# Performance work log

Hardware: AMD Instinct MI355X
Metric: run time of the kernel (lower is better)

Reference implementation:

```python
import jax, jax.numpy as jnp
import numpy as np

NUM_TOP_QUERIES = 300
NUM_CLASSES = 80
CONF_THRESH = 0.0  # with sigmoid scores > 0 always, the mask filter is identity


def setup_inputs() -> dict:
    key = jax.random.key(0)
    k1, k2, k3 = jax.random.split(key, 3)
    N, Q, K = 256, 1000, 80
    logits = jax.random.normal(k1, (N, Q, K), dtype=jnp.float32)
    boxes = jax.random.uniform(k2, (N, Q, 4), dtype=jnp.float32)  # cxcywh in [0,1)
    original_sizes = jax.random.randint(k3, (N, 2), 1, 1333, dtype=jnp.int32)  # (h, w)
    return {"logits": logits, "boxes": boxes, "original_sizes": original_sizes}


def reference(logits, boxes, original_sizes):
    # cxcywh -> xywh (top-left x,y plus w,h)
    cxcy, wh = boxes[..., :2], boxes[..., 2:]
    boxes_xy = jnp.concatenate([cxcy - wh * 0.5, wh], axis=-1)  # (N, Q, 4)

    # NOTE: original module uses only original_sizes[0] for ALL images (faithful)
    hw = original_sizes[0]  # (h, w)
    scale = jnp.concatenate([hw[::-1], hw[::-1]]).astype(boxes.dtype)  # (w, h, w, h)
    boxes_xy = boxes_xy * scale  # (N, Q, 4)

    # sigmoid + topk over flattened (Q*K) class-query scores
    scores = jax.nn.sigmoid(logits).reshape(logits.shape[0], -1)  # (N, Q*K)
    top_scores, index = jax.lax.top_k(scores, NUM_TOP_QUERIES)  # (N, 300)

    labels = index % NUM_CLASSES          # class id
    qidx = index // NUM_CLASSES           # query id

    # gather boxes per top index: (N, 300, 4)
    gathered = jnp.take_along_axis(boxes_xy, qidx[..., None], axis=1)

    all_boxes = jnp.concatenate(
        [labels[..., None].astype(top_scores.dtype), top_scores[..., None], gathered],
        axis=-1,
    )  # (N, 300, 6)

    # Boolean confidence filter. With CONF_THRESH = 0.0 and sigmoid scores,
    # every detection is kept, so the filter+view in the original is identity.
    return all_boxes
```

## Files before the change

kernel.cpp:

```cpp
#include <hip/hip_runtime.h>

#define K_TOP  300
#define NCLS   80
#define NB     256
#define NF4    20000
#define GTHR   2.2f
#define BPB    10
#define CHUNK  2048
#define WPB    4
#define SEGC   96
#define NSEG   (BPB*WPB)
#define NCAND  (NSEG*SEGC)
#define NBK    1024

typedef unsigned int       u32;
typedef unsigned long long u64;

__device__ __forceinline__ u32 order_f32(float f) {
    u32 u = __float_as_uint(f);
    return u ^ ((u >> 31) ? 0xFFFFFFFFu : 0x80000000u);
}
__device__ __forceinline__ float unorder_f32(u32 u) {
    u32 v = (u & 0x80000000u) ? (u ^ 0x80000000u) : ~u;
    return __uint_as_float(v);
}

__device__ __forceinline__ u32 fbucket(u64 key, u32 bias14) {
    u32 d = (u32)(key >> 46) - bias14;
    return (d > 1023u) ? 1023u : d;
}

__device__ __forceinline__ u32 wstore(float v, int idx, u64* __restrict__ seg,
                                      u32 cursor, int lane) {
    const bool win = (v >= GTHR);
    const u64 mask = __ballot(win);
    if (mask) {
        if (win) {
            u32 pos = cursor + (u32)__popcll(mask & ((1ull << lane) - 1ull));
            if (pos < SEGC) {
                u32 o = order_f32(v);
                seg[pos] = ((u64)o << 32) | (u64)(0xFFFFFFFFu - (u32)idx);
            }
        }
        cursor += (u32)__popcll(mask);
    }
    return cursor;
}

__global__ __launch_bounds__(256) void collect_kernel(
    const float* __restrict__ logits,
    u32* __restrict__ gcnt,
    u64* __restrict__ gbuf)
{
    const int blk  = blockIdx.x;
    const int b    = blk & (NB - 1);
    const int c    = blk >> 8;
    const int t    = threadIdx.x;
    const int lane = t & 63;
    const int wseg = (b * BPB + c) * WPB + (t >> 6);

    const float4* __restrict__ L4 = (const float4*)(logits + (size_t)b * (NF4 * 4));
    const int base4 = c * CHUNK;

    float4 v[8];
    if (c < BPB - 1) {
        #pragma unroll
        for (int j = 0; j < 8; ++j) v[j] = L4[base4 + j * 256 + t];
    } else {
        #pragma unroll
        for (int j = 0; j < 8; ++j) {
            const int idx = base4 + j * 256 + t;
            v[j] = (idx < NF4) ? L4[idx]
                               : make_float4(-1e30f, -1e30f, -1e30f, -1e30f);
        }
    }

    u64* __restrict__ seg = gbuf + (size_t)wseg * SEGC;
    u32 cursor = 0;
    #pragma unroll
    for (int j = 0; j < 8; ++j) {
        const int i4 = (base4 + j * 256 + t) * 4;
        cursor = wstore(v[j].x, i4 + 0, seg, cursor, lane);
        cursor = wstore(v[j].y, i4 + 1, seg, cursor, lane);
        cursor = wstore(v[j].z, i4 + 2, seg, cursor, lane);
        cursor = wstore(v[j].w, i4 + 3, seg, cursor, lane);
    }
    if (lane == 0) gcnt[wseg] = cursor;
}


__device__ __forceinline__ void scan1024(u32* hist, u32* cur, u32* wsum,
                                         int* s_B, int t) {
    const int lane = t & 63, w = t >> 6;
    const u32 h = hist[t];
    u32 s = h;
    #pragma unroll
    for (int off = 1; off < 64; off <<= 1) {
        u32 v = (u32)__shfl_down((int)s, off);
        if (lane + off < 64) s += v;
    }
    if (lane == 0) wsum[w] = s;
    __syncthreads();
    u32 wexc = 0;
    #pragma unroll
    for (int j = 0; j < 16; ++j)
        if (j > w) wexc += wsum[j];
    const u32 incl = s + wexc;
    const u32 ex   = incl - h;
    if (incl >= K_TOP) atomicMax(s_B, t);
    hist[t] = ex;
    cur[t]  = ex;
}

__device__ __forceinline__ void rank_and_write(const u64* cand, const u32* hist,
                                               const u32* cur, u32 B, bool fine,
                                               u32 bias14, int t, int b,
                                               const float4* BX, float sx, float sy,
                                               float* out) {
    int total = (int)cur[B]; if (total > NCAND) total = NCAND;
    for (int i = t; i < total; i += 1024) {
        u64 key = cand[i];
        u32 bk  = fine ? fbucket(key, bias14) : (u32)(key >> 54);
        u32 o   = (u32)(key >> 32);
        u32 idx = ~((u32)key);
        int label = (int)(idx % NCLS);
        int q     = (int)(idx / NCLS);
        float4 bx = BX[q];
        int segS = (int)hist[bk];
        int segE = (int)cur[bk]; if (segE > NCAND) segE = NCAND;
        int r = segS;
        for (int j = segS; j < segE; ++j)
            r += (cand[j] > key) ? 1 : 0;
        if (r < K_TOP) {
            float logit = unorder_f32(o);
            float score = 1.0f / (1.0f + expf(-logit));
            float* po = out + ((size_t)b * K_TOP + r) * 6;
            po[0] = (float)label;
            po[1] = score;
            po[2] = (bx.x - 0.5f * bx.z) * sx;
            po[3] = (bx.y - 0.5f * bx.w) * sy;
            po[4] = bx.z * sx;
            po[5] = bx.w * sy;
        }
    }
}

__device__ void full_fallback(const float* __restrict__ logits, int b, int t,
                              u64* cand, u32* hist, u32* cur, u32* wsum, int* s_B,
                              const float4* BX, float sx, float sy,
                              float* __restrict__ out) {
    __syncthreads();
    hist[t] = 0; cur[t] = 0;
    if (t == 0) *s_B = -1;
    __syncthreads();
    const float4* L4 = (const float4*)(logits + (size_t)b * (NF4 * 4));
    for (int i = t; i < NF4; i += 1024) {
        float4 v = L4[i];
        atomicAdd(&hist[order_f32(v.x) >> 22], 1u);
        atomicAdd(&hist[order_f32(v.y) >> 22], 1u);
        atomicAdd(&hist[order_f32(v.z) >> 22], 1u);
        atomicAdd(&hist[order_f32(v.w) >> 22], 1u);
    }
    __syncthreads();
    scan1024(hist, cur, wsum, s_B, t);
    __syncthreads();
    const u32 B = (u32)*s_B;
    for (int i = t; i < NF4; i += 1024) {
        float4 v = L4[i];
        float vv[4] = {v.x, v.y, v.z, v.w};
        #pragma unroll
        for (int u2 = 0; u2 < 4; ++u2) {
            u32 o = order_f32(vv[u2]);
            u32 bk = o >> 22;
            if (bk >= B) {
                u32 pos = atomicAdd(&cur[bk], 1u);
                if (pos < NCAND)
                    cand[pos] = ((u64)o << 32) |
                                (u64)(0xFFFFFFFFu - (u32)(4*i + u2));
            }
        }
    }
    __syncthreads();
    rank_and_write(cand, hist, cur, B, false, 0u, t, b, BX, sx, sy, out);
}

__global__ __launch_bounds__(1024) void select_kernel(
    const float* __restrict__ logits,
    const float* __restrict__ boxes,
    const int*   __restrict__ osz,
    const u32*   __restrict__ gcnt,
    const u64*   __restrict__ gbuf,
    float*       __restrict__ out)
{
    __shared__ u64 cand[NCAND];
    __shared__ u32 hist[NBK];
    __shared__ u32 cur[NBK];
    __shared__ u32 wsum[16];
    __shared__ u32 scc[NSEG];
    __shared__ int s_B;

    const int b = blockIdx.x;
    const int t = threadIdx.x;
    const u64* __restrict__ gb = gbuf + (size_t)b * NCAND;
    const u32 BIAS14 = order_f32(GTHR) >> 14;

    if (t < NSEG) scc[t] = gcnt[b * NSEG + t];
    if (t == 0) s_B = -1;
    hist[t] = 0;
    __syncthreads();

    u64 k0 = 0, k1 = 0, k2 = 0, k3 = 0;
    bool v0 = false, v1 = false, v2 = false, v3 = false;
    {
        const ulonglong2* __restrict__ G2 = (const ulonglong2*)gb;
        ulonglong2 p0 = G2[t];
        int s0 = 2 * t;
        int seg0 = s0 / SEGC;
        int j0   = s0 - seg0 * SEGC;
        k0 = p0.x; k1 = p0.y;
        v0 = (j0     < (int)scc[seg0]);
        v1 = (j0 + 1 < (int)scc[seg0]);
        if (t < 896) {
            ulonglong2 p1 = G2[t + 1024];
            int s2 = 2048 + 2 * t;
            int seg2 = s2 / SEGC;
            int j2   = s2 - seg2 * SEGC;
            k2 = p1.x; k3 = p1.y;
            v2 = (j2     < (int)scc[seg2]);
            v3 = (j2 + 1 < (int)scc[seg2]);
        }
    }

    bool fast = true;
    int total = 0;
    #pragma unroll
    for (int k = 0; k < NSEG; ++k) {
        u32 x = scc[k];
        if (x > SEGC) fast = false; else total += (int)x;
    }
    fast = fast && (total >= K_TOP);

    const float sx = (float)osz[1];
    const float sy = (float)osz[0];
    const float4* BX = (const float4*)(boxes + (size_t)b * 4000);

    if (fast) {
        if (v0) atomicAdd(&hist[fbucket(k0, BIAS14)], 1u);
        if (v1) atomicAdd(&hist[fbucket(k1, BIAS14)], 1u);
        if (v2) atomicAdd(&hist[fbucket(k2, BIAS14)], 1u);
        if (v3) atomicAdd(&hist[fbucket(k3, BIAS14)], 1u);
        __syncthreads();
        scan1024(hist, cur, wsum, &s_B, t);
        __syncthreads();
        fast = (s_B >= 1);
    }

    if (fast) {
        const u32 B = (u32)s_B;
        if (v0) { u32 bk = fbucket(k0, BIAS14);
                  if (bk >= B) { u32 p = atomicAdd(&cur[bk], 1u); cand[p] = k0; } }
        if (v1) { u32 bk = fbucket(k1, BIAS14);
                  if (bk >= B) { u32 p = atomicAdd(&cur[bk], 1u); cand[p] = k1; } }
        if (v2) { u32 bk = fbucket(k2, BIAS14);
                  if (bk >= B) { u32 p = atomicAdd(&cur[bk], 1u); cand[p] = k2; } }
        if (v3) { u32 bk = fbucket(k3, BIAS14);
                  if (bk >= B) { u32 p = atomicAdd(&cur[bk], 1u); cand[p] = k3; } }
        __syncthreads();
        rank_and_write(cand, hist, cur, B, true, BIAS14, t, b, BX, sx, sy, out);
    } else {
        full_fallback(logits, b, t, cand, hist, cur, wsum, &s_B, BX, sx, sy, out);
    }
}

__global__ __launch_bounds__(1024) void select_nows_kernel(
    const float* __restrict__ logits,
    const float* __restrict__ boxes,
    const int*   __restrict__ osz,
    float*       __restrict__ out)
{
    __shared__ u64 cand[NCAND];
    __shared__ u32 hist[NBK];
    __shared__ u32 cur[NBK];
    __shared__ u32 wsum[16];
    __shared__ int s_B;
    const int b = blockIdx.x;
    const int t = threadIdx.x;
    const float sx = (float)osz[1];
    const float sy = (float)osz[0];
    const float4* BX = (const float4*)(boxes + (size_t)b * 4000);
    full_fallback(logits, b, t, cand, hist, cur, wsum, &s_B, BX, sx, sy, out);
}

extern "C" void kernel_launch(void* const* d_in, const int* in_sizes, int n_in,
                              void* d_out, int out_size, void* d_ws, size_t ws_size,
                              hipStream_t stream) {
    const float* logits = (const float*)d_in[0];
    const float* boxes  = (const float*)d_in[1];
    const int*   osz    = (const int*)d_in[2];
    float* out = (float*)d_out;

    const size_t need = 65536 + (size_t)NB * NCAND * sizeof(u64);
    if (ws_size >= need) {
        u32* gcnt = (u32*)d_ws;
        u64* gbuf = (u64*)((char*)d_ws + 65536);
        collect_kernel<<<dim3(NB * BPB), dim3(256), 0, stream>>>(logits, gcnt, gbuf);
        select_kernel<<<dim3(NB), dim3(1024), 0, stream>>>(logits, boxes, osz,
                                                           gcnt, gbuf, out);
    } else {
        select_nows_kernel<<<dim3(NB), dim3(1024), 0, stream>>>(logits, boxes, osz, out);
    }
}
```

Measured before the change: 27.89 us.

## Fuse collect and select into single per-image monolithic kernel

Replaces the two-kernel pipeline (a 2560-block threshold-collect kernel writing candidates to global workspace, then a 256-block select kernel) with one 1024-thread block per image. Each block streams its image's logits itself, keeps threshold survivors in per-wave LDS segments, and then runs the histogram/rank selection directly. This removes the global workspace round-trip and one kernel launch. In exchange only 256 blocks do all the logit reading, which lowers memory-level parallelism, and the extra LDS per block may reduce occupancy.

```diff
diff --git a/kernel.cpp b/kernel.cpp
--- a/kernel.cpp
+++ b/kernel.cpp
@@ -5,12 +5,9 @@
 #define NB     256
 #define NF4    20000
 #define GTHR   2.2f
-#define BPB    10
-#define CHUNK  2048
-#define WPB    4
-#define SEGC   96
-#define NSEG   (BPB*WPB)
-#define NCAND  (NSEG*SEGC)
+#define SEGC   128
+#define NWAVE  16
+#define NCAND  2048
 #define NBK    1024
 
 typedef unsigned int       u32;
@@ -46,48 +43,14 @@
     }
     return cursor;
 }
-
-__global__ __launch_bounds__(256) void collect_kernel(
-    const float* __restrict__ logits,
-    u32* __restrict__ gcnt,
-    u64* __restrict__ gbuf)
-{
-    const int blk  = blockIdx.x;
-    const int b    = blk & (NB - 1);
-    const int c    = blk >> 8;
-    const int t    = threadIdx.x;
-    const int lane = t & 63;
-    const int wseg = (b * BPB + c) * WPB + (t >> 6);
-
-    const float4* __restrict__ L4 = (const float4*)(logits + (size_t)b * (NF4 * 4));
-    const int base4 = c * CHUNK;
-
-    float4 v[8];
-    if (c < BPB - 1) {
-        #pragma unroll
-        for (int j = 0; j < 8; ++j) v[j] = L4[base4 + j * 256 + t];
-    } else {
-        #pragma unroll
-        for (int j = 0; j < 8; ++j) {
-            const int idx = base4 + j * 256 + t;
-            v[j] = (idx < NF4) ? L4[idx]
-                               : make_float4(-1e30f, -1e30f, -1e30f, -1e30f);
-        }
-    }
-
-    u64* __restrict__ seg = gbuf + (size_t)wseg * SEGC;
-    u32 cursor = 0;
-    #pragma unroll
-    for (int j = 0; j < 8; ++j) {
-        const int i4 = (base4 + j * 256 + t) * 4;
-        cursor = wstore(v[j].x, i4 + 0, seg, cursor, lane);
-        cursor = wstore(v[j].y, i4 + 1, seg, cursor, lane);
-        cursor = wstore(v[j].z, i4 + 2, seg, cursor, lane);
-        cursor = wstore(v[j].w, i4 + 3, seg, cursor, lane);
-    }
-    if (lane == 0) gcnt[wseg] = cursor;
-}
-
+__device__ __forceinline__ u32 wstore4(float4 v, int i4, u64* __restrict__ seg,
+                                       u32 cursor, int lane) {
+    cursor = wstore(v.x, i4 + 0, seg, cursor, lane);
+    cursor = wstore(v.y, i4 + 1, seg, cursor, lane);
+    cursor = wstore(v.z, i4 + 2, seg, cursor, lane);
+    cursor = wstore(v.w, i4 + 3, seg, cursor, lane);
+    return cursor;
+}
 
 __device__ __forceinline__ void scan1024(u32* hist, u32* cur, u32* wsum,
                                          int* s_B, int t) {
@@ -184,57 +147,65 @@
     rank_and_write(cand, hist, cur, B, false, 0u, t, b, BX, sx, sy, out);
 }
 
-__global__ __launch_bounds__(1024) void select_kernel(
+__global__ __launch_bounds__(1024) void mono_kernel(
     const float* __restrict__ logits,
     const float* __restrict__ boxes,
     const int*   __restrict__ osz,
-    const u32*   __restrict__ gcnt,
-    const u64*   __restrict__ gbuf,
     float*       __restrict__ out)
 {
+    __shared__ u64 segbuf[NCAND];
     __shared__ u64 cand[NCAND];
     __shared__ u32 hist[NBK];
     __shared__ u32 cur[NBK];
     __shared__ u32 wsum[16];
-    __shared__ u32 scc[NSEG];
+    __shared__ u32 scc[NWAVE];
     __shared__ int s_B;
 
-    const int b = blockIdx.x;
-    const int t = threadIdx.x;
-    const u64* __restrict__ gb = gbuf + (size_t)b * NCAND;
+    const int b    = blockIdx.x;
+    const int t    = threadIdx.x;
+    const int w    = t >> 6;
+    const int lane = t & 63;
     const u32 BIAS14 = order_f32(GTHR) >> 14;
 
-    if (t < NSEG) scc[t] = gcnt[b * NSEG + t];
+    hist[t] = 0;
     if (t == 0) s_B = -1;
-    hist[t] = 0;
-    __syncthreads();
-
-    u64 k0 = 0, k1 = 0, k2 = 0, k3 = 0;
-    bool v0 = false, v1 = false, v2 = false, v3 = false;
+
     {
-        const ulonglong2* __restrict__ G2 = (const ulonglong2*)gb;
-        ulonglong2 p0 = G2[t];
-        int s0 = 2 * t;
-        int seg0 = s0 / SEGC;
-        int j0   = s0 - seg0 * SEGC;
-        k0 = p0.x; k1 = p0.y;
-        v0 = (j0     < (int)scc[seg0]);
-        v1 = (j0 + 1 < (int)scc[seg0]);
-        if (t < 896) {
-            ulonglong2 p1 = G2[t + 1024];
-            int s2 = 2048 + 2 * t;
-            int seg2 = s2 / SEGC;
-            int j2   = s2 - seg2 * SEGC;
-            k2 = p1.x; k3 = p1.y;
-            v2 = (j2     < (int)scc[seg2]);
-            v3 = (j2 + 1 < (int)scc[seg2]);
-        }
-    }
+        const float4* __restrict__ L4 =
+            (const float4*)(logits + (size_t)b * (NF4 * 4));
+        u64* __restrict__ seg = segbuf + w * SEGC;
+        u32 cursor = 0;
+        float4 v[8];
+        #pragma unroll
+        for (int r = 0; r < 8; ++r) v[r] = L4[t + r * 1024];
+        #pragma unroll
+        for (int r = 0; r < 8; ++r)
+            cursor = wstore4(v[r], (t + r * 1024) * 4, seg, cursor, lane);
+        #pragma unroll
+        for (int r = 0; r < 8; ++r) v[r] = L4[t + (8 + r) * 1024];
+        #pragma unroll
+        for (int r = 0; r < 8; ++r)
+            cursor = wstore4(v[r], (t + (8 + r) * 1024) * 4, seg, cursor, lane);
+        float4 a0 = L4[t + 16 * 1024];
+        float4 a1 = L4[t + 17 * 1024];
+        float4 a2 = L4[t + 18 * 1024];
+        cursor = wstore4(a0, (t + 16 * 1024) * 4, seg, cursor, lane);
+        cursor = wstore4(a1, (t + 17 * 1024) * 4, seg, cursor, lane);
+        cursor = wstore4(a2, (t + 18 * 1024) * 4, seg, cursor, lane);
+        if (w <= 8) {
+            const bool tl = (t < 544);
+            float4 a3 = tl ? L4[19456 + t]
+                           : make_float4(-1e30f, -1e30f, -1e30f, -1e30f);
+            cursor = wstore4(a3, (19456 + t) * 4, seg, cursor, lane);
+        }
+        if (lane == 0) scc[w] = cursor;
+    }
+    __syncthreads();
 
     bool fast = true;
     int total = 0;
     #pragma unroll
-    for (int k = 0; k < NSEG; ++k) {
+    for (int k = 0; k < NWAVE; ++k) {
         u32 x = scc[k];
         if (x > SEGC) fast = false; else total += (int)x;
     }
@@ -244,11 +215,20 @@
     const float sy = (float)osz[0];
     const float4* BX = (const float4*)(boxes + (size_t)b * 4000);
 
+    u64 k0, k1;
+    bool v0, v1;
+    {
+        const int sg = t >> 6;
+        const int j  = (2 * t) & 127;
+        k0 = segbuf[2 * t];
+        k1 = segbuf[2 * t + 1];
+        v0 = (j     < (int)scc[sg]);
+        v1 = (j + 1 < (int)scc[sg]);
+    }
+
     if (fast) {
         if (v0) atomicAdd(&hist[fbucket(k0, BIAS14)], 1u);
         if (v1) atomicAdd(&hist[fbucket(k1, BIAS14)], 1u);
-        if (v2) atomicAdd(&hist[fbucket(k2, BIAS14)], 1u);
-        if (v3) atomicAdd(&hist[fbucket(k3, BIAS14)], 1u);
         __syncthreads();
         scan1024(hist, cur, wsum, &s_B, t);
         __syncthreads();
@@ -261,34 +241,11 @@
                   if (bk >= B) { u32 p = atomicAdd(&cur[bk], 1u); cand[p] = k0; } }
         if (v1) { u32 bk = fbucket(k1, BIAS14);
                   if (bk >= B) { u32 p = atomicAdd(&cur[bk], 1u); cand[p] = k1; } }
-        if (v2) { u32 bk = fbucket(k2, BIAS14);
-                  if (bk >= B) { u32 p = atomicAdd(&cur[bk], 1u); cand[p] = k2; } }
-        if (v3) { u32 bk = fbucket(k3, BIAS14);
-                  if (bk >= B) { u32 p = atomicAdd(&cur[bk], 1u); cand[p] = k3; } }
         __syncthreads();
         rank_and_write(cand, hist, cur, B, true, BIAS14, t, b, BX, sx, sy, out);
     } else {
         full_fallback(logits, b, t, cand, hist, cur, wsum, &s_B, BX, sx, sy, out);
     }
-}
-
-__global__ __launch_bounds__(1024) void select_nows_kernel(
-    const float* __restrict__ logits,
-    const float* __restrict__ boxes,
-    const int*   __restrict__ osz,
-    float*       __restrict__ out)
-{
-    __shared__ u64 cand[NCAND];
-    __shared__ u32 hist[NBK];
-    __shared__ u32 cur[NBK];
-    __shared__ u32 wsum[16];
-    __shared__ int s_B;
-    const int b = blockIdx.x;
-    const int t = threadIdx.x;
-    const float sx = (float)osz[1];
-    const float sy = (float)osz[0];
-    const float4* BX = (const float4*)(boxes + (size_t)b * 4000);
-    full_fallback(logits, b, t, cand, hist, cur, wsum, &s_B, BX, sx, sy, out);
 }
 
 extern "C" void kernel_launch(void* const* d_in, const int* in_sizes, int n_in,
@@ -298,15 +255,5 @@
     const float* boxes  = (const float*)d_in[1];
     const int*   osz    = (const int*)d_in[2];
     float* out = (float*)d_out;
-
-    const size_t need = 65536 + (size_t)NB * NCAND * sizeof(u64);
-    if (ws_size >= need) {
-        u32* gcnt = (u32*)d_ws;
-        u64* gbuf = (u64*)((char*)d_ws + 65536);
-        collect_kernel<<<dim3(NB * BPB), dim3(256), 0, stream>>>(logits, gcnt, gbuf);
-        select_kernel<<<dim3(NB), dim3(1024), 0, stream>>>(logits, boxes, osz,
-                                                           gcnt, gbuf, out);
-    } else {
-        select_nows_kernel<<<dim3(NB), dim3(1024), 0, stream>>>(logits, boxes, osz, out);
-    }
-}
+    mono_kernel<<<dim3(NB), dim3(1024), 0, stream>>>(logits, boxes, osz, out);
+}
```

Result: faster. 25.45 us, median of 2 (-8.8%).
